# Performance work log

Hardware: AMD Instinct MI355X
Metric: run time of the kernel (lower is better)

The kernel has to match this reference:

```python
import jax, jax.numpy as jnp
import numpy as np

N1, N2, N3 = 40000, 30000, 30000
N = N1 + N2 + N3          # total nodes after vstack
E = 800000                # edges
D_IN = 256                # in_channels
D_HID = 256               # 2 * out_channels
D_OUT = 128               # out_channels


def _glorot(k, shape):
    lim = (6.0 / (shape[0] + shape[1])) ** 0.5
    return jax.random.uniform(k, shape, jnp.float32, -lim, lim)


def setup_inputs() -> dict:
    key = jax.random.key(0)
    ks = jax.random.split(key, 12)
    x1 = jax.random.normal(ks[0], (N1, 128), jnp.float32)
    x2 = jax.random.normal(ks[1], (N2, 256), jnp.float32)
    x3 = jax.random.normal(ks[2], (N3, 64), jnp.float32)
    edge_index = jax.random.randint(ks[3], (2, E), 0, N, jnp.int64)
    return {
        "x1": x1, "x2": x2, "x3": x3,
        "Wp1": _glorot(ks[4], (128, D_IN)), "bp1": jnp.zeros((D_IN,), jnp.float32),
        "Wp2": _glorot(ks[5], (256, D_IN)), "bp2": jnp.zeros((D_IN,), jnp.float32),
        "Wp3": _glorot(ks[6], (64, D_IN)),  "bp3": jnp.zeros((D_IN,), jnp.float32),
        "W1": _glorot(ks[7], (D_IN, D_HID)), "b1": jnp.zeros((D_HID,), jnp.float32),
        "W2": _glorot(ks[8], (D_HID, D_OUT)), "b2": jnp.zeros((D_OUT,), jnp.float32),
        "edge_index": edge_index,
    }


def _gcn_conv(x, W, b, src, dst, dis):
    # PyG GCNConv: h = xW; out[j] = sum_i norm_ij * h[i] (incl. self-loop) + b
    h = x @ W                                   # [N, d_out]
    msg = h[src] * (dis[src] * dis[dst])[:, None]   # [E, d_out] edge messages
    agg = jax.ops.segment_sum(msg, dst, num_segments=N)
    agg = agg + h * (dis * dis)[:, None]        # self-loop term (norm = 1/deg)
    return agg + b


def reference(x1, x2, x3, Wp1, bp1, Wp2, bp2, Wp3, bp3, W1, b1, W2, b2, edge_index):
    # per-type projection + vstack
    x = jnp.concatenate([x1 @ Wp1 + bp1, x2 @ Wp2 + bp2, x3 @ Wp3 + bp3], axis=0)
    # dropout(p=0.5) is identity in eval mode (deterministic baseline)
    src, dst = edge_index[0], edge_index[1]
    # degree with self-loops (in-degree at dst, as in PyG gcn_norm)
    deg = jnp.ones((N,), x.dtype).at[dst].add(1.0)
    dis = jax.lax.rsqrt(deg)                    # deg^{-1/2}
    h = jax.nn.relu(_gcn_conv(x, W1, b1, src, dst, dis))
    return _gcn_conv(h, W2, b2, src, dst, dis)
```

## Files before the change

kernel.cpp:

```cpp
#include <hip/hip_runtime.h>
#include <cstddef>

#define NT 100000
#define NN1 40000
#define NN2 30000
#define NN3 30000
#define EE 800000

typedef _Float16 f16;
typedef f16 f16x8 __attribute__((ext_vector_type(8)));
typedef f16 f16x4 __attribute__((ext_vector_type(4)));
typedef float f32x4 __attribute__((ext_vector_type(4)));

static inline int cdiv(int a, int b) { return (a + b - 1) / b; }

__device__ __forceinline__ void gload_lds16(const f16* g, f16* l) {
    __builtin_amdgcn_global_load_lds(
        (const __attribute__((address_space(1))) void*)g,
        (__attribute__((address_space(3))) void*)l, 16, 0, 0);
}

__global__ void k_scan1(const int* __restrict__ cnt, int* __restrict__ rowptr,
                        int* __restrict__ part, float* __restrict__ dis, int n) {
    __shared__ int sums[256];
    int b = blockIdx.x, t = threadIdx.x;
    int base = b * 1024 + t * 4;
    int v0 = (base + 0 < n) ? cnt[base + 0] : 0;
    int v1 = (base + 1 < n) ? cnt[base + 1] : 0;
    int v2 = (base + 2 < n) ? cnt[base + 2] : 0;
    int v3 = (base + 3 < n) ? cnt[base + 3] : 0;
    if (base + 0 < n) dis[base + 0] = rsqrtf((float)v0 + 1.0f);
    if (base + 1 < n) dis[base + 1] = rsqrtf((float)v1 + 1.0f);
    if (base + 2 < n) dis[base + 2] = rsqrtf((float)v2 + 1.0f);
    if (base + 3 < n) dis[base + 3] = rsqrtf((float)v3 + 1.0f);
    int tsum = v0 + v1 + v2 + v3;
    sums[t] = tsum;
    __syncthreads();
    for (int off = 1; off < 256; off <<= 1) {
        int y = (t >= off) ? sums[t - off] : 0;
        __syncthreads();
        sums[t] += y;
        __syncthreads();
    }
    int excl = sums[t] - tsum;
    if (base + 0 < n) rowptr[base + 0] = excl;
    if (base + 1 < n) rowptr[base + 1] = excl + v0;
    if (base + 2 < n) rowptr[base + 2] = excl + v0 + v1;
    if (base + 3 < n) rowptr[base + 3] = excl + v0 + v1 + v2;
    if (t == 255) part[b] = sums[255];
}

__global__ void k_scan2(int* __restrict__ part, int nb) {
    __shared__ int sums[256];
    int t = threadIdx.x;
    int v = (t < nb) ? part[t] : 0;
    sums[t] = v;
    __syncthreads();
    for (int off = 1; off < 256; off <<= 1) {
        int y = (t >= off) ? sums[t - off] : 0;
        __syncthreads();
        sums[t] += y;
        __syncthreads();
    }
    if (t < nb) part[t] = sums[t] - v;
}

__global__ void k_scan3(int* __restrict__ rowptr, const int* __restrict__ part,
                        int n, int total) {
    int i = blockIdx.x * blockDim.x + threadIdx.x;
    if (i < n) rowptr[i] += part[i >> 10];
    if (i == 0) rowptr[n] = total;
}

struct TArgs {
    const float *W0, *W1, *W2, *W3, *W4;
    f16 *T0, *T1, *T2, *T3, *T4;
};
#define HB   3125
#define CVTB 14375
#define TRB  832
#define NA4  1280000
#define NB4  1920000
#define NC4  480000
struct PrepArgs {
    const int* dst; int* cnt;
    const float *x1, *x2, *x3; f16* xc;
    TArgs t;
};
__global__ __launch_bounds__(256) void k_prep(PrepArgs a) {
    int bid = blockIdx.x, tid = threadIdx.x;
    if (bid < HB) {
        int i = bid * 256 + tid;
        if (i < EE) atomicAdd(&a.cnt[a.dst[i]], 1);
    } else if (bid < HB + CVTB) {
        int i = (bid - HB) * 256 + tid;
        const float* s; int j;
        if (i < NA4) { s = a.x1; j = i; }
        else if (i < NA4 + NB4) { s = a.x2; j = i - NA4; }
        else if (i < NA4 + NB4 + NC4) { s = a.x3; j = i - NA4 - NB4; }
        else return;
        float4 v = reinterpret_cast<const float4*>(s)[j];
        f16x4 r = {(f16)v.x, (f16)v.y, (f16)v.z, (f16)v.w};
        reinterpret_cast<f16x4*>(a.xc)[i] = r;
    } else {
        int i = (bid - HB - CVTB) * 256 + tid;
        const float* W; f16* T; int K, N, j;
        if      (i <  32768) { W = a.t.W0; T = a.t.T0; K = 128; N = 256; j = i; }
        else if (i <  98304) { W = a.t.W1; T = a.t.T1; K = 256; N = 256; j = i - 32768; }
        else if (i < 114688) { W = a.t.W2; T = a.t.T2; K =  64; N = 256; j = i - 98304; }
        else if (i < 180224) { W = a.t.W3; T = a.t.T3; K = 256; N = 256; j = i - 114688; }
        else if (i < 212992) { W = a.t.W4; T = a.t.T4; K = 256; N = 128; j = i - 180224; }
        else return;
        int k = j / N, n = j - k * N;
        T[n * K + k] = (f16)W[j];
    }
}

template<bool RELU_OUT, bool HAS_BIAS>
__device__ __forceinline__
void hgemm_body(f16* As, f16* Bs,
                const f16* __restrict__ A, const f16* __restrict__ BT,
                const float* __restrict__ bias, f16* __restrict__ C,
                int M, int K, int N, int bx, int by) {
    const int tid = threadIdx.x;
    const int lane = tid & 63;
    const int wid = tid >> 6;
    const int wm = wid & 1, wn = wid >> 1;
    const int bm = bx * 128;
    const int bn = by * 128;
    const int r15 = lane & 15, g = lane >> 4;
    const int sr  = lane >> 2;
    const int chs = (lane & 3) ^ ((lane >> 3) & 3);

    auto stage = [&](int buf, int k0) {
        #pragma unroll
        for (int q = 0; q < 2; ++q) {
            int chunk = wid + q * 4;
            int row = chunk * 16 + sr;
            int ga = bm + row; if (ga >= M) ga = M - 1;
            gload_lds16(A  + (size_t)ga * K + k0 + chs * 8, As + buf * 4096 + chunk * 512);
            gload_lds16(BT + (size_t)(bn + row) * K + k0 + chs * 8, Bs + buf * 4096 + chunk * 512);
        }
    };

    f32x4 acc[4][4] = {};
    const int nsteps = K >> 5;
    stage(0, 0);
    __syncthreads();
    int cur = 0;
    for (int step = 0; step < nsteps; ++step) {
        if (step + 1 < nsteps) stage(cur ^ 1, (step + 1) << 5);
        f16x8 af[4], bf[4];
        const int sl = (g ^ ((r15 >> 1) & 3)) * 8;
        #pragma unroll
        for (int mf = 0; mf < 4; ++mf) {
            int row = wm * 64 + mf * 16 + r15;
            af[mf] = *reinterpret_cast<const f16x8*>(As + cur * 4096 + row * 32 + sl);
        }
        #pragma unroll
        for (int nf = 0; nf < 4; ++nf) {
            int row = wn * 64 + nf * 16 + r15;
            bf[nf] = *reinterpret_cast<const f16x8*>(Bs + cur * 4096 + row * 32 + sl);
        }
        #pragma unroll
        for (int mf = 0; mf < 4; ++mf)
            #pragma unroll
            for (int nf = 0; nf < 4; ++nf)
                acc[mf][nf] = __builtin_amdgcn_mfma_f32_16x16x32_f16(af[mf], bf[nf], acc[mf][nf], 0, 0, 0);
        __syncthreads();
        cur ^= 1;
    }

    #pragma unroll
    for (int mf = 0; mf < 4; ++mf) {
        #pragma unroll
        for (int nf = 0; nf < 4; ++nf) {
            int col = bn + wn * 64 + nf * 16 + r15;
            float bv = HAS_BIAS ? bias[col] : 0.f;
            #pragma unroll
            for (int r = 0; r < 4; ++r) {
                int rowg = bm + wm * 64 + mf * 16 + g * 4 + r;
                if (rowg < M) {
                    float v = acc[mf][nf][r] + bv;
                    if (RELU_OUT) v = fmaxf(v, 0.f);
                    C[(size_t)rowg * N + col] = (f16)v;
                }
            }
        }
    }
}

struct P3 {
    const f16 *a1, *a2, *a3, *t1, *t2, *t3;
    const float *b1, *b2, *b3;
    f16 *o1, *o2, *o3;
    int g1, g2;
};
#define FB 3125
struct FPArgs {
    const int *src, *dst;
    const float* dis;
    const int* rowptr;
    int* cursor;
    int2* e_pairs;
    P3 p;
};
__global__ __launch_bounds__(256) void k_fillproj(FPArgs a) {
    extern __shared__ f16 smem[];
    int bid = blockIdx.x;
    if (bid < FB) {
        int i = bid * 256 + threadIdx.x;
        if (i >= EE) return;
        int s = a.src[i], t = a.dst[i];
        int pos = atomicAdd(&a.cursor[t], 1);
        int2 pr;
        pr.x = s;
        pr.y = __float_as_int(a.dis[s] * a.dis[t]);
        a.e_pairs[a.rowptr[t] + pos] = pr;
    } else {
        int pb = bid - FB;
        int bx = pb >> 1, by = pb & 1;
        if (bx < a.p.g1)
            hgemm_body<false, true>(smem, smem + 8192, a.p.a1, a.p.t1, a.p.b1, a.p.o1, NN1, 128, 256, bx, by);
        else if (bx < a.p.g1 + a.p.g2)
            hgemm_body<false, true>(smem, smem + 8192, a.p.a2, a.p.t2, a.p.b2, a.p.o2, NN2, 256, 256, bx - a.p.g1, by);
        else
            hgemm_body<false, true>(smem, smem + 8192, a.p.a3, a.p.t3, a.p.b3, a.p.o3, NN3, 64, 256, bx - a.p.g1 - a.p.g2, by);
    }
}

__global__ __launch_bounds__(512)
void k_fused(const f16* __restrict__ x16, const float* __restrict__ dis,
             const int* __restrict__ rowptr, const int2* __restrict__ e_pairs,
             const f16* __restrict__ W1T, const float* __restrict__ b1,
             const f16* __restrict__ W2T, f16* __restrict__ hw2, int M) {
    __shared__ f16 P[64 * 256];
    const int tid = threadIdx.x;
    const int lane = tid & 63;
    const int bm = blockIdx.x * 64;

    {
        const int grp = tid >> 5;
        const int l = tid & 31;
        #pragma unroll
        for (int it = 0; it < 4; ++it) {
            int row = it * 16 + grp;
            int node = bm + row;
            float av[8];
            if (node < M) {
                float dj = dis[node];
                int r0 = rowptr[node], r1 = rowptr[node + 1];
                int deg = r1 - r0;
                int si = 0; float wi = 0.f;
                if (l < deg) { int2 pr = e_pairs[r0 + l]; si = pr.x; wi = __int_as_float(pr.y); }
                f16x8 sa = reinterpret_cast<const f16x8*>(x16 + (size_t)node * 256)[l];
                float wself = dj * dj;
                #pragma unroll
                for (int k = 0; k < 8; ++k) av[k] = (float)sa[k] * wself;
                int n32 = deg < 32 ? deg : 32;
                int e = 0;
                for (; e + 4 <= n32; e += 4) {
                    int s0 = __shfl(si, e + 0, 32), s1 = __shfl(si, e + 1, 32);
                    int s2 = __shfl(si, e + 2, 32), s3 = __shfl(si, e + 3, 32);
                    float w0 = __shfl(wi, e + 0, 32), w1 = __shfl(wi, e + 1, 32);
                    float w2 = __shfl(wi, e + 2, 32), w3 = __shfl(wi, e + 3, 32);
                    f16x8 u0 = reinterpret_cast<const f16x8*>(x16 + (size_t)s0 * 256)[l];
                    f16x8 u1 = reinterpret_cast<const f16x8*>(x16 + (size_t)s1 * 256)[l];
                    f16x8 u2 = reinterpret_cast<const f16x8*>(x16 + (size_t)s2 * 256)[l];
                    f16x8 u3 = reinterpret_cast<const f16x8*>(x16 + (size_t)s3 * 256)[l];
                    #pragma unroll
                    for (int k = 0; k < 8; ++k)
                        av[k] += (float)u0[k] * w0 + (float)u1[k] * w1
                               + (float)u2[k] * w2 + (float)u3[k] * w3;
                }
                for (; e < n32; ++e) {
                    int s0 = __shfl(si, e, 32);
                    float w0 = __shfl(wi, e, 32);
                    f16x8 u0 = reinterpret_cast<const f16x8*>(x16 + (size_t)s0 * 256)[l];
                    #pragma unroll
                    for (int k = 0; k < 8; ++k) av[k] += (float)u0[k] * w0;
                }
                for (int e2 = r0 + 32; e2 < r1; ++e2) {
                    int2 pr = e_pairs[e2];
                    float w0 = __int_as_float(pr.y);
                    f16x8 u0 = reinterpret_cast<const f16x8*>(x16 + (size_t)pr.x * 256)[l];
                    #pragma unroll
                    for (int k = 0; k < 8; ++k) av[k] += (float)u0[k] * w0;
                }
            } else {
                #pragma unroll
                for (int k = 0; k < 8; ++k) av[k] = 0.f;
            }
            f16x8 r;
            #pragma unroll
            for (int k = 0; k < 8; ++k) r[k] = (f16)av[k];
            int slot = (l & 3) ^ ((row >> 1) & 3);
            *reinterpret_cast<f16x8*>(P + (l >> 2) * 2048 + row * 32 + slot * 8) = r;
        }
    }
    __syncthreads();

    const int w = tid >> 6;
    const int r15 = lane & 15, g = lane >> 4;
    f32x4 acc[4][2] = {};
    for (int step = 0; step < 8; ++step) {
        f16x8 af[4], bf[2];
        #pragma unroll
        for (int mf = 0; mf < 4; ++mf) {
            int row = mf * 16 + r15;
            int slot = g ^ ((row >> 1) & 3);
            af[mf] = *reinterpret_cast<const f16x8*>(P + step * 2048 + row * 32 + slot * 8);
        }
        #pragma unroll
        for (int nf = 0; nf < 2; ++nf) {
            int n1 = w * 32 + nf * 16 + r15;
            bf[nf] = *reinterpret_cast<const f16x8*>(W1T + (size_t)n1 * 256 + step * 32 + g * 8);
        }
        #pragma unroll
        for (int mf = 0; mf < 4; ++mf)
            #pragma unroll
            for (int nf = 0; nf < 2; ++nf)
                acc[mf][nf] = __builtin_amdgcn_mfma_f32_16x16x32_f16(af[mf], bf[nf], acc[mf][nf], 0, 0, 0);
    }
    __syncthreads();

    #pragma unroll
    for (int nf = 0; nf < 2; ++nf) {
        int col = w * 32 + nf * 16 + r15;
        float bv = b1[col];
        int gp = (col >> 3) & 3, c7 = col & 7;
        #pragma unroll
        for (int mf = 0; mf < 4; ++mf) {
            #pragma unroll
            for (int rr = 0; rr < 4; ++rr) {
                int row = mf * 16 + g * 4 + rr;
                float v = fmaxf(acc[mf][nf][rr] + bv, 0.f);
                int slot = gp ^ ((row >> 1) & 3);
                P[w * 2048 + row * 32 + slot * 8 + c7] = (f16)v;
            }
        }
    }
    __syncthreads();

    f32x4 acc2[4] = {};
    for (int step = 0; step < 8; ++step) {
        f16x8 af[4], bf;
        #pragma unroll
        for (int mf = 0; mf < 4; ++mf) {
            int row = mf * 16 + r15;
            int slot = g ^ ((row >> 1) & 3);
            af[mf] = *reinterpret_cast<const f16x8*>(P + step * 2048 + row * 32 + slot * 8);
        }
        int n2 = w * 16 + r15;
        bf = *reinterpret_cast<const f16x8*>(W2T + (size_t)n2 * 256 + step * 32 + g * 8);
        #pragma unroll
        for (int mf = 0; mf < 4; ++mf)
            acc2[mf] = __builtin_amdgcn_mfma_f32_16x16x32_f16(af[mf], bf, acc2[mf], 0, 0, 0);
    }

    #pragma unroll
    for (int mf = 0; mf < 4; ++mf) {
        int col = w * 16 + r15;
        #pragma unroll
        for (int rr = 0; rr < 4; ++rr) {
            int rowg = bm + mf * 16 + g * 4 + rr;
            if (rowg < M)
                hw2[(size_t)rowg * 128 + col] = (f16)acc2[mf][rr];
        }
    }
}

__global__ void k_gather128(const f16* __restrict__ f, const float* __restrict__ dis,
                            const int* __restrict__ rowptr, const int2* __restrict__ e_pairs,
                            const float* __restrict__ bias, float* __restrict__ outb, int n) {
    int node = (int)(((long long)blockIdx.x * blockDim.x + threadIdx.x) >> 5);
    int l = threadIdx.x & 31;
    if (node >= n) return;
    float dj = dis[node];
    int r0 = rowptr[node], r1 = rowptr[node + 1];
    int deg = r1 - r0;
    int si = 0; float wi = 0.f;
    if (l < deg) { int2 p = e_pairs[r0 + l]; si = p.x; wi = __int_as_float(p.y); }
    f16x4 a = reinterpret_cast<const f16x4*>(f + (size_t)node * 128)[l];
    float wsf = dj * dj;
    float acc[4];
    #pragma unroll
    for (int k = 0; k < 4; ++k) acc[k] = (float)a[k] * wsf;
    int n32 = deg < 32 ? deg : 32;
    int e = 0;
    for (; e + 8 <= n32; e += 8) {
        int s[8]; float w[8];
        #pragma unroll
        for (int q = 0; q < 8; ++q) {
            s[q] = __shfl(si, e + q, 32);
            w[q] = __shfl(wi, e + q, 32);
        }
        f16x4 u[8];
        #pragma unroll
        for (int q = 0; q < 8; ++q)
            u[q] = reinterpret_cast<const f16x4*>(f + (size_t)s[q] * 128)[l];
        #pragma unroll
        for (int q = 0; q < 8; ++q)
            #pragma unroll
            for (int k = 0; k < 4; ++k) acc[k] += (float)u[q][k] * w[q];
    }
    for (; e + 4 <= n32; e += 4) {
        int s[4]; float w[4];
        #pragma unroll
        for (int q = 0; q < 4; ++q) {
            s[q] = __shfl(si, e + q, 32);
            w[q] = __shfl(wi, e + q, 32);
        }
        f16x4 u[4];
        #pragma unroll
        for (int q = 0; q < 4; ++q)
            u[q] = reinterpret_cast<const f16x4*>(f + (size_t)s[q] * 128)[l];
        #pragma unroll
        for (int q = 0; q < 4; ++q)
            #pragma unroll
            for (int k = 0; k < 4; ++k) acc[k] += (float)u[q][k] * w[q];
    }
    for (; e < n32; ++e) {
        int s0 = __shfl(si, e, 32);
        float w0 = __shfl(wi, e, 32);
        f16x4 u0 = reinterpret_cast<const f16x4*>(f + (size_t)s0 * 128)[l];
        #pragma unroll
        for (int k = 0; k < 4; ++k) acc[k] += (float)u0[k] * w0;
    }
    for (int e2 = r0 + 32; e2 < r1; ++e2) {
        int2 p = e_pairs[e2];
        float w0 = __int_as_float(p.y);
        f16x4 u0 = reinterpret_cast<const f16x4*>(f + (size_t)p.x * 128)[l];
        #pragma unroll
        for (int k = 0; k < 4; ++k) acc[k] += (float)u0[k] * w0;
    }
    float4 bb = reinterpret_cast<const float4*>(bias)[l];
    float4 r = make_float4(acc[0] + bb.x, acc[1] + bb.y, acc[2] + bb.z, acc[3] + bb.w);
    reinterpret_cast<float4*>(outb + (size_t)node * 128)[l] = r;
}

extern "C" void kernel_launch(void* const* d_in, const int* in_sizes, int n_in,
                              void* d_out, int out_size, void* d_ws, size_t ws_size,
                              hipStream_t stream) {
    const float* x1  = (const float*)d_in[0];
    const float* x2  = (const float*)d_in[1];
    const float* x3  = (const float*)d_in[2];
    const float* Wp1 = (const float*)d_in[3];
    const float* bp1 = (const float*)d_in[4];
    const float* Wp2 = (const float*)d_in[5];
    const float* bp2 = (const float*)d_in[6];
    const float* Wp3 = (const float*)d_in[7];
    const float* bp3 = (const float*)d_in[8];
    const float* W1  = (const float*)d_in[9];
    const float* b1  = (const float*)d_in[10];
    const float* W2  = (const float*)d_in[11];
    const float* b2  = (const float*)d_in[12];
    const int*   ei  = (const int*)d_in[13];
    const int* src = ei;
    const int* dst = ei + EE;
    float* out = (float*)d_out;

    char* ws = (char*)d_ws;
    size_t off = 0;
    auto alloc = [&](size_t bytes) {
        char* p = ws + off;
        off += (bytes + 511) & ~(size_t)511;
        return p;
    };
    float* dis    = (float*)alloc((size_t)NT * 4);
    int*   cnt    = (int*)alloc((size_t)NT * 4);
    int*   cursor = (int*)alloc((size_t)NT * 4);
    int*   rowptr = (int*)alloc((size_t)(NT + 1) * 4);
    int*   part   = (int*)alloc(256 * 4);
    int2*  e_pairs= (int2*)alloc((size_t)EE * 8);
    f16*   x16    = (f16*)alloc((size_t)NT * 256 * 2);
    f16*   hw216  = (f16*)alloc((size_t)NT * 128 * 2);
    f16*   xc     = (f16*)alloc((size_t)(NN1 * 128 + NN2 * 256 + NN3 * 64) * 2);
    f16*   Wp1T   = (f16*)alloc((size_t)256 * 128 * 2);
    f16*   Wp2T   = (f16*)alloc((size_t)256 * 256 * 2);
    f16*   Wp3T   = (f16*)alloc((size_t)256 * 64 * 2);
    f16*   W1T    = (f16*)alloc((size_t)256 * 256 * 2);
    f16*   W2T    = (f16*)alloc((size_t)128 * 256 * 2);

    f16* x1c = xc;
    f16* x2c = xc + (size_t)NN1 * 128;
    f16* x3c = xc + (size_t)NN1 * 128 + (size_t)NN2 * 256;

    const int nb = cdiv(NT, 1024);

    size_t zspan = (size_t)((char*)rowptr - (char*)cnt);
    hipMemsetAsync(cnt, 0, zspan, stream);

    {
        PrepArgs a;
        a.dst = dst; a.cnt = cnt;
        a.x1 = x1; a.x2 = x2; a.x3 = x3; a.xc = xc;
        a.t = {Wp1, Wp2, Wp3, W1, W2, Wp1T, Wp2T, Wp3T, W1T, W2T};
        k_prep<<<HB + CVTB + TRB, 256, 0, stream>>>(a);
    }

    k_scan1<<<nb, 256, 0, stream>>>(cnt, rowptr, part, dis, NT);
    k_scan2<<<1, 256, 0, stream>>>(part, nb);
    k_scan3<<<cdiv(NT, 256), 256, 0, stream>>>(rowptr, part, NT, EE);

    {
        FPArgs a;
        a.src = src; a.dst = dst; a.dis = dis; a.rowptr = rowptr;
        a.cursor = cursor; a.e_pairs = e_pairs;
        a.p = {x1c, x2c, x3c, Wp1T, Wp2T, Wp3T, bp1, bp2, bp3,
               x16, x16 + (size_t)NN1 * 256, x16 + (size_t)(NN1 + NN2) * 256,
               cdiv(NN1, 128), cdiv(NN2, 128)};
        int projb = (cdiv(NN1, 128) + cdiv(NN2, 128) + cdiv(NN3, 128)) * 2;
        k_fillproj<<<FB + projb, 256, 32768, stream>>>(a);
    }

    k_fused<<<cdiv(NT, 64), 512, 0, stream>>>(x16, dis, rowptr, e_pairs,
                                              W1T, b1, W2T, hw216, NT);

    k_gather128<<<cdiv(NT * 32, 256), 256, 0, stream>>>(hw216, dis, rowptr, e_pairs, b2, out, NT);
}
```

Baseline: 272.0 us.

## Merge scan kernels and interleave two-row gather prologue in fused GCN kernel

Each block of a single merged kernel now redundantly scans the per-block partial sums and applies the offsets, which removes one kernel launch. The fused layer-1 kernel processes rows in pairs and issues the rowptr, dis, self-feature and edge-list loads for both rows before either gather loop starts. The intent is to overlap memory latency across the two rows. The launch bound now asks for 8 waves per EU, which may cap registers and cause spills. Out-of-range rows are clamped to the last node and zeroed at the write instead of being branched around.

```diff
diff --git a/kernel.cpp b/kernel.cpp
--- a/kernel.cpp
+++ b/kernel.cpp
@@ -50,25 +50,25 @@
     if (t == 255) part[b] = sums[255];
 }
 
-__global__ void k_scan2(int* __restrict__ part, int nb) {
-    __shared__ int sums[256];
+__global__ void k_scan23(int* __restrict__ rowptr, const int* __restrict__ part,
+                         int n, int total, int nb) {
+    __shared__ int ps[256];
     int t = threadIdx.x;
     int v = (t < nb) ? part[t] : 0;
-    sums[t] = v;
+    ps[t] = v;
     __syncthreads();
     for (int off = 1; off < 256; off <<= 1) {
-        int y = (t >= off) ? sums[t - off] : 0;
+        int y = (t >= off) ? ps[t - off] : 0;
         __syncthreads();
-        sums[t] += y;
+        ps[t] += y;
         __syncthreads();
     }
-    if (t < nb) part[t] = sums[t] - v;
-}
-
-__global__ void k_scan3(int* __restrict__ rowptr, const int* __restrict__ part,
-                        int n, int total) {
-    int i = blockIdx.x * blockDim.x + threadIdx.x;
-    if (i < n) rowptr[i] += part[i >> 10];
+    int incl = ps[t];
+    __syncthreads();
+    ps[t] = incl - v;
+    __syncthreads();
+    int i = blockIdx.x * blockDim.x + t;
+    if (i < n) rowptr[i] += ps[i >> 10];
     if (i == 0) rowptr[n] = total;
 }
 
@@ -229,7 +229,7 @@
     }
 }
 
-__global__ __launch_bounds__(512)
+__global__ __launch_bounds__(512, 8)
 void k_fused(const f16* __restrict__ x16, const float* __restrict__ dis,
              const int* __restrict__ rowptr, const int2* __restrict__ e_pairs,
              const f16* __restrict__ W1T, const float* __restrict__ b1,
@@ -243,27 +243,34 @@
         const int grp = tid >> 5;
         const int l = tid & 31;
         #pragma unroll
-        for (int it = 0; it < 4; ++it) {
-            int row = it * 16 + grp;
-            int node = bm + row;
-            float av[8];
-            if (node < M) {
-                float dj = dis[node];
-                int r0 = rowptr[node], r1 = rowptr[node + 1];
-                int deg = r1 - r0;
-                int si = 0; float wi = 0.f;
-                if (l < deg) { int2 pr = e_pairs[r0 + l]; si = pr.x; wi = __int_as_float(pr.y); }
-                f16x8 sa = reinterpret_cast<const f16x8*>(x16 + (size_t)node * 256)[l];
-                float wself = dj * dj;
+        for (int half = 0; half < 2; ++half) {
+            const int rowA = (half * 2 + 0) * 16 + grp;
+            const int rowB = (half * 2 + 1) * 16 + grp;
+            const int ndA = bm + rowA, ndB = bm + rowB;
+            const bool okA = ndA < M, okB = ndB < M;
+            const int ncA = okA ? ndA : M - 1, ncB = okB ? ndB : M - 1;
+            int r0A = rowptr[ncA], r1A = rowptr[ncA + 1];
+            int r0B = rowptr[ncB], r1B = rowptr[ncB + 1];
+            float djA = dis[ncA], djB = dis[ncB];
+            f16x8 saA = reinterpret_cast<const f16x8*>(x16 + (size_t)ncA * 256)[l];
+            f16x8 saB = reinterpret_cast<const f16x8*>(x16 + (size_t)ncB * 256)[l];
+            int degA = r1A - r0A, degB = r1B - r0B;
+            int siA = 0, siB = 0; float wiA = 0.f, wiB = 0.f;
+            if (l < degA) { int2 pr = e_pairs[r0A + l]; siA = pr.x; wiA = __int_as_float(pr.y); }
+            if (l < degB) { int2 pr = e_pairs[r0B + l]; siB = pr.x; wiB = __int_as_float(pr.y); }
+
+            {
+                float av[8];
+                float wself = djA * djA;
                 #pragma unroll
-                for (int k = 0; k < 8; ++k) av[k] = (float)sa[k] * wself;
-                int n32 = deg < 32 ? deg : 32;
+                for (int k = 0; k < 8; ++k) av[k] = (float)saA[k] * wself;
+                int n32 = degA < 32 ? degA : 32;
                 int e = 0;
                 for (; e + 4 <= n32; e += 4) {
-                    int s0 = __shfl(si, e + 0, 32), s1 = __shfl(si, e + 1, 32);
-                    int s2 = __shfl(si, e + 2, 32), s3 = __shfl(si, e + 3, 32);
-                    float w0 = __shfl(wi, e + 0, 32), w1 = __shfl(wi, e + 1, 32);
-                    float w2 = __shfl(wi, e + 2, 32), w3 = __shfl(wi, e + 3, 32);
+                    int s0 = __shfl(siA, e + 0, 32), s1 = __shfl(siA, e + 1, 32);
+                    int s2 = __shfl(siA, e + 2, 32), s3 = __shfl(siA, e + 3, 32);
+                    float w0 = __shfl(wiA, e + 0, 32), w1 = __shfl(wiA, e + 1, 32);
+                    float w2 = __shfl(wiA, e + 2, 32), w3 = __shfl(wiA, e + 3, 32);
                     f16x8 u0 = reinterpret_cast<const f16x8*>(x16 + (size_t)s0 * 256)[l];
                     f16x8 u1 = reinterpret_cast<const f16x8*>(x16 + (size_t)s1 * 256)[l];
                     f16x8 u2 = reinterpret_cast<const f16x8*>(x16 + (size_t)s2 * 256)[l];
@@ -274,28 +281,66 @@
                                + (float)u2[k] * w2 + (float)u3[k] * w3;
                 }
                 for (; e < n32; ++e) {
-                    int s0 = __shfl(si, e, 32);
-                    float w0 = __shfl(wi, e, 32);
+                    int s0 = __shfl(siA, e, 32);
+                    float w0 = __shfl(wiA, e, 32);
                     f16x8 u0 = reinterpret_cast<const f16x8*>(x16 + (size_t)s0 * 256)[l];
                     #pragma unroll
                     for (int k = 0; k < 8; ++k) av[k] += (float)u0[k] * w0;
                 }
-                for (int e2 = r0 + 32; e2 < r1; ++e2) {
+                for (int e2 = r0A + 32; e2 < r1A; ++e2) {
                     int2 pr = e_pairs[e2];
                     float w0 = __int_as_float(pr.y);
                     f16x8 u0 = reinterpret_cast<const f16x8*>(x16 + (size_t)pr.x * 256)[l];
                     #pragma unroll
                     for (int k = 0; k < 8; ++k) av[k] += (float)u0[k] * w0;
                 }
-            } else {
+                f16x8 r;
                 #pragma unroll
-                for (int k = 0; k < 8; ++k) av[k] = 0.f;
+                for (int k = 0; k < 8; ++k) r[k] = okA ? (f16)av[k] : (f16)0.f;
+                int slot = (l & 3) ^ ((rowA >> 1) & 3);
+                *reinterpret_cast<f16x8*>(P + (l >> 2) * 2048 + rowA * 32 + slot * 8) = r;
             }
-            f16x8 r;
-            #pragma unroll
-            for (int k = 0; k < 8; ++k) r[k] = (f16)av[k];
-            int slot = (l & 3) ^ ((row >> 1) & 3);
-            *reinterpret_cast<f16x8*>(P + (l >> 2) * 2048 + row * 32 + slot * 8) = r;
+            {
+                float av[8];
+                float wself = djB * djB;
+                #pragma unroll
+                for (int k = 0; k < 8; ++k) av[k] = (float)saB[k] * wself;
+                int n32 = degB < 32 ? degB : 32;
+                int e = 0;
+                for (; e + 4 <= n32; e += 4) {
+                    int s0 = __shfl(siB, e + 0, 32), s1 = __shfl(siB, e + 1, 32);
+                    int s2 = __shfl(siB, e + 2, 32), s3 = __shfl(siB, e + 3, 32);
+                    float w0 = __shfl(wiB, e + 0, 32), w1 = __shfl(wiB, e + 1, 32);
+                    float w2 = __shfl(wiB, e + 2, 32), w3 = __shfl(wiB, e + 3, 32);
+                    f16x8 u0 = reinterpret_cast<const f16x8*>(x16 + (size_t)s0 * 256)[l];
+                    f16x8 u1 = reinterpret_cast<const f16x8*>(x16 + (size_t)s1 * 256)[l];
+                    f16x8 u2 = reinterpret_cast<const f16x8*>(x16 + (size_t)s2 * 256)[l];
+                    f16x8 u3 = reinterpret_cast<const f16x8*>(x16 + (size_t)s3 * 256)[l];
+                    #pragma unroll
+                    for (int k = 0; k < 8; ++k)
+                        av[k] += (float)u0[k] * w0 + (float)u1[k] * w1
+                               + (float)u2[k] * w2 + (float)u3[k] * w3;
+                }
+                for (; e < n32; ++e) {
+                    int s0 = __shfl(siB, e, 32);
+                    float w0 = __shfl(wiB, e, 32);
+                    f16x8 u0 = reinterpret_cast<const f16x8*>(x16 + (size_t)s0 * 256)[l];
+                    #pragma unroll
+                    for (int k = 0; k < 8; ++k) av[k] += (float)u0[k] * w0;
+                }
+                for (int e2 = r0B + 32; e2 < r1B; ++e2) {
+                    int2 pr = e_pairs[e2];
+                    float w0 = __int_as_float(pr.y);
+                    f16x8 u0 = reinterpret_cast<const f16x8*>(x16 + (size_t)pr.x * 256)[l];
+                    #pragma unroll
+                    for (int k = 0; k < 8; ++k) av[k] += (float)u0[k] * w0;
+                }
+                f16x8 r;
+                #pragma unroll
+                for (int k = 0; k < 8; ++k) r[k] = okB ? (f16)av[k] : (f16)0.f;
+                int slot = (l & 3) ^ ((rowB >> 1) & 3);
+                *reinterpret_cast<f16x8*>(P + (l >> 2) * 2048 + rowB * 32 + slot * 8) = r;
+            }
         }
     }
     __syncthreads();
@@ -500,8 +545,7 @@
     }
 
     k_scan1<<<nb, 256, 0, stream>>>(cnt, rowptr, part, dis, NT);
-    k_scan2<<<1, 256, 0, stream>>>(part, nb);
-    k_scan3<<<cdiv(NT, 256), 256, 0, stream>>>(rowptr, part, NT, EE);
+    k_scan23<<<cdiv(NT, 256), 256, 0, stream>>>(rowptr, part, NT, EE, nb);
 
     {
         FPArgs a;
```

Measured after the change: 274.9 us. Within noise of the previous version (+1.1%).
